# Performance work log

Hardware: AMD Instinct MI355X
Metric: run time of the kernel (lower is better)

The kernel has to match this reference:

```python
import jax, jax.numpy as jnp
import numpy as np

EPS = 1e-5

def setup_inputs() -> dict:
    key = jax.random.key(0)
    k1, k2, k3, k4, k5 = jax.random.split(key, 5)
    B, D, S = 4096, 2048, 16384
    return {
        "x": jax.random.normal(k1, (B, D), dtype=jnp.float32),
        "W_enc": jax.random.normal(k2, (S, D), dtype=jnp.float32) * 0.02,  # encoder.weight [n_sae, n_input]
        "W_dec": jax.random.normal(k3, (D, S), dtype=jnp.float32) * 0.02,  # decoder.weight [n_input, n_sae]
        "pre_bias": jax.random.normal(k4, (D,), dtype=jnp.float32) * 0.01,
        "sae_bias": jax.random.normal(k5, (S,), dtype=jnp.float32) * 0.01,
        "k": 64,
    }

def reference(x, W_enc, W_dec, pre_bias, sae_bias, k):
    # --- pre_process: layer norm (torch.std is unbiased -> ddof=1) ---
    x_mean = jnp.mean(x, axis=-1, keepdims=True)
    std = jnp.std(x, axis=-1, ddof=1, keepdims=True)
    x_ln = (x - x_mean) / (std + EPS)
    # --- encode: latents_pre = (x_ln - pre_bias) @ W_enc^T + sae_bias ---
    pre_activations = (x_ln - pre_bias) @ W_enc.T + sae_bias  # [B, n_sae]
    # --- TopK activation: keep top-k, ReLU them, zero the rest ---
    vals, idx = jax.lax.top_k(pre_activations, k)              # [B, k]
    vals = jax.nn.relu(vals)
    rows = jnp.arange(pre_activations.shape[0])[:, None]       # [B, 1]
    latents = jnp.zeros_like(pre_activations).at[rows, idx].set(vals)
    # --- decode + un-normalize ---
    recons = latents @ W_dec.T + pre_bias                      # [B, n_input]
    recons = recons * std + x_mean
    return pre_activations, latents, recons
```

## Files before the change

kernel.cpp:

```cpp
#include <hip/hip_runtime.h>
#include <cstdint>
#include <cstddef>

#define EPSV 1e-5f
#define CAP 224
#define PAD 16
#define DELTA 0.02f
#define AMBCAP 64

__device__ __forceinline__ unsigned short f2bf(float f) {
  unsigned u = __float_as_uint(f);
  unsigned r = (u + 0x7FFFu + ((u >> 16) & 1u)) >> 16;
  return (unsigned short)r;
}
__device__ __forceinline__ float bf2f(unsigned short h) {
  return __uint_as_float(((unsigned)h) << 16);
}

__global__ __launch_bounds__(256) void ln_kernel(const float* __restrict__ x,
    const float* __restrict__ pre_bias, float* __restrict__ a,
    unsigned short* __restrict__ A2,
    float* __restrict__ stats, int D) {
  const int b = blockIdx.x;
  const int tid = threadIdx.x;
  const float4* x4 = reinterpret_cast<const float4*>(x + (size_t)b * D);
  const float4* pb4 = reinterpret_cast<const float4*>(pre_bias);
  float4* a4 = reinterpret_cast<float4*>(a + (size_t)b * D);
  float4 v0 = x4[tid], v1 = x4[tid + 256];
  float s = v0.x + v0.y + v0.z + v0.w + v1.x + v1.y + v1.z + v1.w;
  float ss = v0.x*v0.x + v0.y*v0.y + v0.z*v0.z + v0.w*v0.w
           + v1.x*v1.x + v1.y*v1.y + v1.z*v1.z + v1.w*v1.w;
#pragma unroll
  for (int off = 1; off < 64; off <<= 1) { s += __shfl_xor(s, off); ss += __shfl_xor(ss, off); }
  __shared__ float wsum[4], wssq[4], bmean, bstd;
  int wave = tid >> 6;
  if ((tid & 63) == 0) { wsum[wave] = s; wssq[wave] = ss; }
  __syncthreads();
  if (tid == 0) {
    float S1 = wsum[0] + wsum[1] + wsum[2] + wsum[3];
    float S2 = wssq[0] + wssq[1] + wssq[2] + wssq[3];
    float mean = S1 / (float)D;
    float var = (S2 - (float)D * mean * mean) / (float)(D - 1);
    float sd = sqrtf(fmaxf(var, 0.f));
    bmean = mean; bstd = sd;
    stats[2*b] = mean; stats[2*b+1] = sd;
  }
  __syncthreads();
  float mean = bmean, rstd = 1.f / (bstd + EPSV);
  float4 p0 = pb4[tid], p1 = pb4[tid + 256];
  float4 o0, o1;
  o0.x = (v0.x - mean) * rstd - p0.x; o0.y = (v0.y - mean) * rstd - p0.y;
  o0.z = (v0.z - mean) * rstd - p0.z; o0.w = (v0.w - mean) * rstd - p0.w;
  o1.x = (v1.x - mean) * rstd - p1.x; o1.y = (v1.y - mean) * rstd - p1.y;
  o1.z = (v1.z - mean) * rstd - p1.z; o1.w = (v1.w - mean) * rstd - p1.w;
  a4[tid] = o0; a4[tid + 256] = o1;
  if (A2) {
    unsigned short* row = A2 + (size_t)b * 2048;
    ushort4 h0 = make_ushort4(f2bf(o0.x), f2bf(o0.y), f2bf(o0.z), f2bf(o0.w));
    ushort4 h1 = make_ushort4(f2bf(o1.x), f2bf(o1.y), f2bf(o1.z), f2bf(o1.w));
    *reinterpret_cast<ushort4*>(row + tid * 4) = h0;
    *reinterpret_cast<ushort4*>(row + 1024 + tid * 4) = h1;
  }
}

__global__ __launch_bounds__(256) void cvt_w_kernel(const float* __restrict__ W,
    unsigned short* __restrict__ W2, int D) {
  const int s = blockIdx.x, tid = threadIdx.x;
  const float4* w4 = reinterpret_cast<const float4*>(W + (size_t)s * D);
  unsigned short* row = W2 + (size_t)s * D;
  float4 v0 = w4[tid * 2], v1 = w4[tid * 2 + 1];
  uint4 p;
  p.x = (unsigned)f2bf(v0.x) | ((unsigned)f2bf(v0.y) << 16);
  p.y = (unsigned)f2bf(v0.z) | ((unsigned)f2bf(v0.w) << 16);
  p.z = (unsigned)f2bf(v1.x) | ((unsigned)f2bf(v1.y) << 16);
  p.w = (unsigned)f2bf(v1.z) | ((unsigned)f2bf(v1.w) << 16);
  *reinterpret_cast<uint4*>(row + tid * 8) = p;
}

typedef __attribute__((ext_vector_type(8))) short bf8;
typedef __attribute__((ext_vector_type(4))) float f32x4;

__device__ __forceinline__ void gload16(const void* g, void* l) {
  __builtin_amdgcn_global_load_lds(
      (const __attribute__((address_space(1))) unsigned int*)g,
      (__attribute__((address_space(3))) unsigned int*)l,
      16, 0, 0);
}

__global__ __launch_bounds__(256) void enc_gemm_bf16(
    const unsigned short* __restrict__ A2,
    const unsigned short* __restrict__ W2,
    const float* __restrict__ sae_bias,
    float* __restrict__ C, int M, int N) {
  __shared__ __align__(16) short As[128 * 64];
  __shared__ __align__(16) short Bs[128 * 64];
  const int tid = threadIdx.x;
  const int bn = blockIdx.x, bm = blockIdx.y;
  const int w = tid >> 6, l = tid & 63;

  const int lrow = l >> 3;
  const int lcol = ((l & 7) ^ lrow) * 8;
  const unsigned short* gA[4];
  const unsigned short* gB[4];
#pragma unroll
  for (int i = 0; i < 4; ++i) {
    int chunk = w * 4 + i;
    int row = chunk * 8 + lrow;
    gA[i] = A2 + (size_t)(bm * 128 + row) * 2048 + lcol;
    gB[i] = W2 + (size_t)(bn * 128 + row) * 2048 + lcol;
  }

  const int wm = (w >> 1) * 64, wn = (w & 1) * 64;
  const int r15 = l & 15, b7 = l & 7, u = l >> 4;
  const int colks0 = ((u + 0) ^ b7) * 8;
  const int colks1 = ((u + 4) ^ b7) * 8;
  const int baseA = (wm + r15) * 64;
  const int baseB = (wn + r15) * 64;

  f32x4 acc[4][4];
#pragma unroll
  for (int mi = 0; mi < 4; ++mi)
#pragma unroll
    for (int ni = 0; ni < 4; ++ni) acc[mi][ni] = (f32x4){0.f, 0.f, 0.f, 0.f};

  for (int t = 0; t < 32; ++t) {
    int koff = t * 64;
#pragma unroll
    for (int i = 0; i < 4; ++i) {
      int chunk = w * 4 + i;
      gload16(gA[i] + koff, &As[chunk * 512]);
      gload16(gB[i] + koff, &Bs[chunk * 512]);
    }
    __syncthreads();
#pragma unroll
    for (int ks = 0; ks < 2; ++ks) {
      const int ck = ks ? colks1 : colks0;
      bf8 af[4], bfv[4];
#pragma unroll
      for (int mi = 0; mi < 4; ++mi)
        af[mi] = *reinterpret_cast<const bf8*>(&As[baseA + mi * 1024 + ck]);
#pragma unroll
      for (int ni = 0; ni < 4; ++ni)
        bfv[ni] = *reinterpret_cast<const bf8*>(&Bs[baseB + ni * 1024 + ck]);
#pragma unroll
      for (int mi = 0; mi < 4; ++mi)
#pragma unroll
        for (int ni = 0; ni < 4; ++ni)
          acc[mi][ni] = __builtin_amdgcn_mfma_f32_16x16x32_bf16(
              af[mi], bfv[ni], acc[mi][ni], 0, 0, 0);
    }
    __syncthreads();
  }

  const int cm = (l >> 4) * 4, cn = l & 15;
  float sb[4];
#pragma unroll
  for (int ni = 0; ni < 4; ++ni)
    sb[ni] = sae_bias[bn * 128 + wn + ni * 16 + cn];
#pragma unroll
  for (int mi = 0; mi < 4; ++mi) {
#pragma unroll
    for (int r = 0; r < 4; ++r) {
      int row = bm * 128 + wm + mi * 16 + cm + r;
      float* Crow = C + (size_t)row * N + bn * 128 + wn;
#pragma unroll
      for (int ni = 0; ni < 4; ++ni)
        Crow[ni * 16 + cn] = acc[mi][ni][r] + sb[ni];
    }
  }
}

#define BM 128
#define BN 128
#define BK 32
#define LDP 136

__global__ __launch_bounds__(256) void enc_gemm_f32(
    const float* __restrict__ A, const float* __restrict__ Bw,
    const float* __restrict__ sae_bias, float* __restrict__ C,
    int M, int N, int K) {
  __shared__ __align__(16) float As[BK * LDP];
  __shared__ __align__(16) float Bs[BK * LDP];
  const int tid = threadIdx.x;
  const int bn = blockIdx.x, bm = blockIdx.y;
  const float* Ab = A + (size_t)bm * BM * K;
  const float* Bb = Bw + (size_t)bn * BN * K;
  float acc[8][8];
#pragma unroll
  for (int i = 0; i < 8; ++i)
#pragma unroll
    for (int j = 0; j < 8; ++j) acc[i][j] = 0.f;
  const int tn = tid & 15, tm = tid >> 4;
  const int lk = tid & 31;
  const int lm4 = (tid >> 5) * 4;
  for (int k0 = 0; k0 < K; k0 += BK) {
#pragma unroll
    for (int i = 0; i < 4; ++i) {
      int mb = i * 32 + lm4;
      float a0 = Ab[(size_t)(mb + 0) * K + k0 + lk];
      float a1 = Ab[(size_t)(mb + 1) * K + k0 + lk];
      float a2 = Ab[(size_t)(mb + 2) * K + k0 + lk];
      float a3 = Ab[(size_t)(mb + 3) * K + k0 + lk];
      *reinterpret_cast<float4*>(&As[lk * LDP + mb]) = make_float4(a0, a1, a2, a3);
      float b0 = Bb[(size_t)(mb + 0) * K + k0 + lk];
      float b1 = Bb[(size_t)(mb + 1) * K + k0 + lk];
      float b2 = Bb[(size_t)(mb + 2) * K + k0 + lk];
      float b3 = Bb[(size_t)(mb + 3) * K + k0 + lk];
      *reinterpret_cast<float4*>(&Bs[lk * LDP + mb]) = make_float4(b0, b1, b2, b3);
    }
    __syncthreads();
#pragma unroll 8
    for (int kk = 0; kk < BK; ++kk) {
      float4 a0 = *reinterpret_cast<const float4*>(&As[kk * LDP + tm * 4]);
      float4 a1 = *reinterpret_cast<const float4*>(&As[kk * LDP + tm * 4 + 64]);
      float4 b0 = *reinterpret_cast<const float4*>(&Bs[kk * LDP + tn * 4]);
      float4 b1 = *reinterpret_cast<const float4*>(&Bs[kk * LDP + tn * 4 + 64]);
      float av[8] = {a0.x, a0.y, a0.z, a0.w, a1.x, a1.y, a1.z, a1.w};
      float bv[8] = {b0.x, b0.y, b0.z, b0.w, b1.x, b1.y, b1.z, b1.w};
#pragma unroll
      for (int ii = 0; ii < 8; ++ii)
#pragma unroll
        for (int jj = 0; jj < 8; ++jj)
          acc[ii][jj] = fmaf(av[ii], bv[jj], acc[ii][jj]);
    }
    __syncthreads();
  }
  float4 sb0 = *reinterpret_cast<const float4*>(sae_bias + bn * BN + tn * 4);
  float4 sb1 = *reinterpret_cast<const float4*>(sae_bias + bn * BN + tn * 4 + 64);
#pragma unroll
  for (int ii = 0; ii < 8; ++ii) {
    int row = bm * BM + (ii < 4 ? tm * 4 + ii : 64 + tm * 4 + ii - 4);
    float* Crow = C + (size_t)row * N + bn * BN;
    float4 o0 = make_float4(acc[ii][0] + sb0.x, acc[ii][1] + sb0.y,
                            acc[ii][2] + sb0.z, acc[ii][3] + sb0.w);
    float4 o1 = make_float4(acc[ii][4] + sb1.x, acc[ii][5] + sb1.y,
                            acc[ii][6] + sb1.z, acc[ii][7] + sb1.w);
    *reinterpret_cast<float4*>(Crow + tn * 4) = o0;
    *reinterpret_cast<float4*>(Crow + tn * 4 + 64) = o1;
  }
}

__device__ __forceinline__ unsigned mapf(float f) {
  unsigned u = __float_as_uint(f);
  return (u & 0x80000000u) ? ~u : (u | 0x80000000u);
}

__global__ __launch_bounds__(256) void topk_select(
    const float* __restrict__ preact, float* __restrict__ latents,
    const int* __restrict__ kp, int* __restrict__ cand, float* __restrict__ candv,
    int* __restrict__ candcnt, int S) {
  const int b = blockIdx.x, tid = threadIdx.x;
  const float4* row4 = reinterpret_cast<const float4*>(preact + (size_t)b * S);
  __shared__ int hist[4096];
  __shared__ int tsum[256];
  __shared__ unsigned sh_pref, sh_thr;
  __shared__ int sh_done, sh_cum, sh_cnt;
  int K = kp[0]; if (K > 192) K = 192;
  const int r = K + PAD;
  if (tid == 0) { sh_done = 0; sh_pref = 0; sh_cum = 0; }
  for (int level = 0; level < 3; ++level) {
    __syncthreads();
    if (sh_done) break;
    const int shift = (level == 0) ? 20 : (level == 1) ? 8 : 0;
    const int width = (level == 2) ? 8 : 12;
    const int nb = 1 << width;
    const unsigned mask = (unsigned)nb - 1;
    for (int i = tid; i < nb; i += 256) hist[i] = 0;
    __syncthreads();
    const unsigned pref = sh_pref;
    for (int i = tid; i < S / 4; i += 256) {
      float4 v = row4[i];
      unsigned uu[4] = {mapf(v.x), mapf(v.y), mapf(v.z), mapf(v.w)};
#pragma unroll
      for (int q = 0; q < 4; ++q) {
        bool ok = (level == 0) || ((uu[q] >> (shift + width)) == pref);
        if (ok) atomicAdd(&hist[(uu[q] >> shift) & mask], 1);
      }
    }
    __syncthreads();
    const int per = nb >> 8;
    int myts = 0;
#pragma unroll 4
    for (int j = 0; j < per; ++j) myts += hist[tid * per + j];
    tsum[tid] = myts;
    __syncthreads();
    for (int o = 1; o < 256; o <<= 1) {
      int v_ = (tid + o < 256) ? tsum[tid + o] : 0;
      __syncthreads();
      tsum[tid] += v_;
      __syncthreads();
    }
    const int rr = r - sh_cum;
    const int sufIncl = tsum[tid];
    const int sufExcl = sufIncl - myts;
    if (sufExcl < rr && rr <= sufIncl) {
      int running = sufExcl;
      for (int j = per - 1; j >= 0; --j) {
        int bb = tid * per + j;
        int c = hist[bb];
        if (running + c >= rr) {
          unsigned npref = (sh_pref << width) | (unsigned)bb;
          int candTotal = sh_cum + running + c;
          sh_pref = npref;
          sh_cum += running;
          if (candTotal <= CAP || level == 2) { sh_thr = npref << shift; sh_done = 1; }
          break;
        }
        running += c;
      }
    }
  }
  __syncthreads();
  const unsigned T = sh_thr;
  if (tid == 0) sh_cnt = 0;
  __syncthreads();
  float4* lat4 = reinterpret_cast<float4*>(latents + (size_t)b * S);
  float4 z = make_float4(0.f, 0.f, 0.f, 0.f);
  for (int i = tid; i < S / 4; i += 256) {
    float4 v = row4[i];
    unsigned uu[4] = {mapf(v.x), mapf(v.y), mapf(v.z), mapf(v.w)};
    float vv[4] = {v.x, v.y, v.z, v.w};
#pragma unroll
    for (int q = 0; q < 4; ++q) {
      if (uu[q] >= T) {
        int p = atomicAdd(&sh_cnt, 1);
        if (p < CAP) { cand[(size_t)b * CAP + p] = i * 4 + q; candv[(size_t)b * CAP + p] = vv[q]; }
      }
    }
    lat4[i] = z;
  }
  __syncthreads();
  if (tid == 0) candcnt[b] = (sh_cnt < CAP) ? sh_cnt : CAP;
}

__global__ __launch_bounds__(256) void topk_refine(
    const float* __restrict__ a, const float* __restrict__ W_enc,
    const float* __restrict__ sae_bias, const int* __restrict__ kp,
    const int* __restrict__ cand, const float* __restrict__ candv,
    const int* __restrict__ candcnt,
    float* __restrict__ latents, int* __restrict__ out_idx, float* __restrict__ out_val,
    int D, int S) {
  const int b = blockIdx.x, tid = threadIdx.x;
  __shared__ float sv[256];
  __shared__ int si[256];
  __shared__ double sv64[256];
  __shared__ double av[AMBCAP];
  __shared__ int aslot[AMBCAP], agid[AMBCAP];
  __shared__ int sh_amb, sh_nin;
  int K = kp[0]; if (K > 192) K = 192;
  const int cnt = candcnt[b];
  const int wave = tid >> 6, lane = tid & 63;
  const float4* ar4 = reinterpret_cast<const float4*>(a + (size_t)b * D);
  const int nit = D / 256;

  if (tid < cnt) { sv[tid] = candv[(size_t)b * CAP + tid]; si[tid] = cand[(size_t)b * CAP + tid]; }
  else { sv[tid] = -3.0e38f; si[tid] = 0x7FFFFFFF; }
  __syncthreads();
  for (int ksz = 2; ksz <= 256; ksz <<= 1) {
    for (int j = ksz >> 1; j > 0; j >>= 1) {
      int ixj = tid ^ j;
      if (ixj > tid) {
        float v1 = sv[tid], v2 = sv[ixj];
        int i1 = si[tid], i2 = si[ixj];
        bool dirDesc = ((tid & ksz) == 0);
        bool firstBetter = (v1 > v2) || (v1 == v2 && i1 < i2);
        if (dirDesc ? (!firstBetter) : firstBetter) {
          sv[tid] = v2; sv[ixj] = v1; si[tid] = i2; si[ixj] = i1;
        }
      }
      __syncthreads();
    }
  }
  const float vK = sv[K - 1];
  if (tid == 0) { sh_amb = 0; sh_nin = 0; }
  __syncthreads();
  bool isC = tid < cnt;
  if (isC && (sv[tid] > vK + DELTA)) atomicAdd(&sh_nin, 1);
  if (isC && fabsf(sv[tid] - vK) <= DELTA) {
    int p = atomicAdd(&sh_amb, 1);
    if (p < AMBCAP) { aslot[p] = tid; agid[p] = si[tid]; }
  }
  __syncthreads();
  const int nAmb = sh_amb, nIn = sh_nin;

  if (nAmb <= AMBCAP) {
    for (int c = wave; c < nAmb; c += 4) {
      int sidx = agid[c];
      const float4* wr4 = reinterpret_cast<const float4*>(W_enc + (size_t)sidx * D);
      double acc = 0.0;
      for (int m = 0; m < nit; ++m) {
        float4 a_ = ar4[m * 64 + lane];
        float4 w_ = wr4[m * 64 + lane];
        acc += (double)a_.x * w_.x + (double)a_.y * w_.y
             + (double)a_.z * w_.z + (double)a_.w * w_.w;
      }
#pragma unroll
      for (int off = 1; off < 64; off <<= 1) acc += __shfl_xor(acc, off);
      if (lane == 0) av[c] = acc + (double)sae_bias[sidx];
    }
    __syncthreads();
    if (tid < AMBCAP && tid >= nAmb) { av[tid] = -1.0e300; agid[tid] = 0x7FFFFFFF; }
    __syncthreads();
    for (int ksz = 2; ksz <= AMBCAP; ksz <<= 1) {
      for (int j = ksz >> 1; j > 0; j >>= 1) {
        int ixj = tid ^ j;
        if (tid < AMBCAP && ixj > tid) {
          double v1 = av[tid], v2 = av[ixj];
          int i1 = agid[tid], i2 = agid[ixj];
          bool dirDesc = ((tid & ksz) == 0);
          bool firstBetter = (v1 > v2) || (v1 == v2 && i1 < i2);
          if (dirDesc ? (!firstBetter) : firstBetter) {
            av[tid] = v2; av[ixj] = v1; agid[tid] = i2; agid[ixj] = i1;
          }
        }
        __syncthreads();
      }
    }
    if (tid < K) {
      int gidx; float val;
      if (tid < nIn) { gidx = si[tid]; val = sv[tid]; }
      else { int c = tid - nIn; gidx = agid[c]; val = (float)av[c]; }
      val = fmaxf(val, 0.f);
      latents[(size_t)b * S + gidx] = val;
      out_idx[(size_t)b * 256 + tid] = gidx;
      out_val[(size_t)b * 256 + tid] = val;
    }
  } else {
    for (int c = wave; c < cnt; c += 4) {
      int sidx = si[c];
      const float4* wr4 = reinterpret_cast<const float4*>(W_enc + (size_t)sidx * D);
      double acc = 0.0;
      for (int m = 0; m < nit; ++m) {
        float4 a_ = ar4[m * 64 + lane];
        float4 w_ = wr4[m * 64 + lane];
        acc += (double)a_.x * w_.x + (double)a_.y * w_.y
             + (double)a_.z * w_.z + (double)a_.w * w_.w;
      }
#pragma unroll
      for (int off = 1; off < 64; off <<= 1) acc += __shfl_xor(acc, off);
      if (lane == 0) sv64[c] = acc + (double)sae_bias[sidx];
    }
    __syncthreads();
    if (tid >= cnt) { sv64[tid] = -1.0e300; si[tid] = 0x7FFFFFFF; }
    __syncthreads();
    for (int ksz = 2; ksz <= 256; ksz <<= 1) {
      for (int j = ksz >> 1; j > 0; j >>= 1) {
        int ixj = tid ^ j;
        if (ixj > tid) {
          double v1 = sv64[tid], v2 = sv64[ixj];
          int i1 = si[tid], i2 = si[ixj];
          bool dirDesc = ((tid & ksz) == 0);
          bool firstBetter = (v1 > v2) || (v1 == v2 && i1 < i2);
          if (dirDesc ? (!firstBetter) : firstBetter) {
            sv64[tid] = v2; sv64[ixj] = v1; si[tid] = i2; si[ixj] = i1;
          }
        }
        __syncthreads();
      }
    }
    if (tid < K) {
      int idx = si[tid];
      float rv = fmaxf((float)sv64[tid], 0.f);
      latents[(size_t)b * S + idx] = rv;
      out_idx[(size_t)b * 256 + tid] = idx;
      out_val[(size_t)b * 256 + tid] = rv;
    }
  }
}

__global__ __launch_bounds__(256) void transpose_cvt(const float* __restrict__ src,
    unsigned short* __restrict__ dst, int D, int S) {
  __shared__ float t[32][33];
  int s0 = blockIdx.x * 32, d0 = blockIdx.y * 32;
  int tx = threadIdx.x & 31, ty = threadIdx.x >> 5;
#pragma unroll
  for (int i = 0; i < 32; i += 8)
    t[ty + i][tx] = src[(size_t)(d0 + ty + i) * S + s0 + tx];
  __syncthreads();
#pragma unroll
  for (int i = 0; i < 32; i += 8)
    dst[(size_t)(s0 + ty + i) * D + d0 + tx] = f2bf(t[tx][ty + i]);
}

__global__ __launch_bounds__(256) void decode_bf16(
    const unsigned short* __restrict__ WdTh, const float* __restrict__ pre_bias,
    const float* __restrict__ stats, const int* __restrict__ kp,
    const int* __restrict__ out_idx, const float* __restrict__ out_val,
    float* __restrict__ recons, int D) {
  const int b = blockIdx.x, tid = threadIdx.x;
  __shared__ int sidx[192];
  __shared__ float sval[192];
  int K = kp[0]; if (K > 192) K = 192;
  if (tid < K) { sidx[tid] = out_idx[(size_t)b * 256 + tid]; sval[tid] = out_val[(size_t)b * 256 + tid]; }
  __syncthreads();
  const int c0 = tid * 8;
  float4 p0 = *reinterpret_cast<const float4*>(pre_bias + c0);
  float4 p1 = *reinterpret_cast<const float4*>(pre_bias + c0 + 4);
  float acc[8] = {p0.x, p0.y, p0.z, p0.w, p1.x, p1.y, p1.z, p1.w};
  for (int j = 0; j < K; ++j) {
    float v = sval[j];
    uint4 wv = *reinterpret_cast<const uint4*>(WdTh + (size_t)sidx[j] * D + c0);
    acc[0] = fmaf(v, bf2f((unsigned short)(wv.x & 0xffff)), acc[0]);
    acc[1] = fmaf(v, bf2f((unsigned short)(wv.x >> 16)),    acc[1]);
    acc[2] = fmaf(v, bf2f((unsigned short)(wv.y & 0xffff)), acc[2]);
    acc[3] = fmaf(v, bf2f((unsigned short)(wv.y >> 16)),    acc[3]);
    acc[4] = fmaf(v, bf2f((unsigned short)(wv.z & 0xffff)), acc[4]);
    acc[5] = fmaf(v, bf2f((unsigned short)(wv.z >> 16)),    acc[5]);
    acc[6] = fmaf(v, bf2f((unsigned short)(wv.w & 0xffff)), acc[6]);
    acc[7] = fmaf(v, bf2f((unsigned short)(wv.w >> 16)),    acc[7]);
  }
  float mean = stats[2 * b], sd = stats[2 * b + 1];
  float4 o0 = make_float4(acc[0] * sd + mean, acc[1] * sd + mean,
                          acc[2] * sd + mean, acc[3] * sd + mean);
  float4 o1 = make_float4(acc[4] * sd + mean, acc[5] * sd + mean,
                          acc[6] * sd + mean, acc[7] * sd + mean);
  float* r = recons + (size_t)b * D + c0;
  *reinterpret_cast<float4*>(r) = o0;
  *reinterpret_cast<float4*>(r + 4) = o1;
}

__global__ __launch_bounds__(256) void decode_fb(
    const float* __restrict__ Wd, const float* __restrict__ pre_bias,
    const float* __restrict__ stats, const int* __restrict__ kp,
    const int* __restrict__ out_idx, const float* __restrict__ out_val,
    float* __restrict__ recons, int D, int S) {
  const int b = blockIdx.x, tid = threadIdx.x;
  __shared__ int sidx[192];
  __shared__ float sval[192];
  int K = kp[0]; if (K > 192) K = 192;
  if (tid < K) { sidx[tid] = out_idx[(size_t)b * 256 + tid]; sval[tid] = out_val[(size_t)b * 256 + tid]; }
  __syncthreads();
  for (int d = tid; d < D; d += 256) {
    float acc = pre_bias[d];
    for (int j = 0; j < K; ++j)
      acc = fmaf(sval[j], Wd[(size_t)d * S + sidx[j]], acc);
    recons[(size_t)b * D + d] = acc * stats[2 * b + 1] + stats[2 * b];
  }
}

extern "C" void kernel_launch(void* const* d_in, const int* in_sizes, int n_in,
                              void* d_out, int out_size, void* d_ws, size_t ws_size,
                              hipStream_t stream) {
  const float* x        = (const float*)d_in[0];
  const float* W_enc    = (const float*)d_in[1];
  const float* W_dec    = (const float*)d_in[2];
  const float* pre_bias = (const float*)d_in[3];
  const float* sae_bias = (const float*)d_in[4];
  const int*   kp       = (const int*)d_in[5];
  const int D = in_sizes[3];
  const int S = in_sizes[4];
  const int B = in_sizes[0] / D;

  float* out_pre = (float*)d_out;
  float* out_lat = out_pre + (size_t)B * S;
  float* out_rec = out_lat + (size_t)B * S;

  char* ws = (char*)d_ws;
  size_t off = 0;
  float* a = (float*)(ws + off);        off += (size_t)B * D * 4;
  float* stats = (float*)(ws + off);    off += (size_t)B * 2 * 4;
  int* cand = (int*)(ws + off);         off += (size_t)B * CAP * 4;
  float* candv = (float*)(ws + off);    off += (size_t)B * CAP * 4;
  int* candcnt = (int*)(ws + off);      off += (size_t)B * 4;
  int* oidx = (int*)(ws + off);         off += (size_t)B * 256 * 4;
  float* oval = (float*)(ws + off);     off += (size_t)B * 256 * 4;
  off = (off + 255) & ~(size_t)255;
  unsigned short* A2 = (unsigned short*)(ws + off);
  size_t offW2 = off + (size_t)B * D * 2;
  unsigned short* W2 = (unsigned short*)(ws + offW2);
  size_t offWdT = offW2 + (size_t)S * D * 2;
  unsigned short* WdTh = (unsigned short*)(ws + offWdT);
  size_t offEnd = offWdT + (size_t)S * D * 2;
  bool useBf16 = (D == 2048) && (B % 128 == 0) && (S % 128 == 0) &&
                 (S % 32 == 0) && (D % 32 == 0) && (ws_size >= offEnd);

  if (useBf16) {
    ln_kernel<<<B, 256, 0, stream>>>(x, pre_bias, a, A2, stats, D);
    cvt_w_kernel<<<S, 256, 0, stream>>>(W_enc, W2, D);
    enc_gemm_bf16<<<dim3(S / 128, B / 128), 256, 0, stream>>>(A2, W2, sae_bias, out_pre, B, S);
    transpose_cvt<<<dim3(S / 32, D / 32), 256, 0, stream>>>(W_dec, WdTh, D, S);
    topk_select<<<B, 256, 0, stream>>>(out_pre, out_lat, kp, cand, candv, candcnt, S);
    topk_refine<<<B, 256, 0, stream>>>(a, W_enc, sae_bias, kp, cand, candv, candcnt,
                                       out_lat, oidx, oval, D, S);
    decode_bf16<<<B, 256, 0, stream>>>(WdTh, pre_bias, stats, kp, oidx, oval, out_rec, D);
  } else {
    ln_kernel<<<B, 256, 0, stream>>>(x, pre_bias, a, nullptr, stats, D);
    enc_gemm_f32<<<dim3(S / BN, B / BM), 256, 0, stream>>>(a, W_enc, sae_bias, out_pre, B, S, D);
    topk_select<<<B, 256, 0, stream>>>(out_pre, out_lat, kp, cand, candv, candcnt, S);
    topk_refine<<<B, 256, 0, stream>>>(a, W_enc, sae_bias, kp, cand, candv, candcnt,
                                       out_lat, oidx, oval, D, S);
    decode_fb<<<B, 256, 0, stream>>>(W_dec, pre_bias, stats, kp, oidx, oval, out_rec, D, S);
  }
}
```

Baseline: 916.9 us.

## Double-buffer LDS tiles in encoder GEMM to overlap global loads with MFMA

The encoder bf16 GEMM now uses two LDS buffer pairs. It issues the global-to-LDS loads for the next K tile before computing on the current one, so load latency overlaps with MFMA work and each tile needs only one barrier instead of two. It also raises wave priority around the MFMA block with s_setprio. The cost is doubled LDS use (64KB per block), which may reduce occupancy, and the explicit vmcnt(0) wait plus barrier must order the buffer reuse correctly.

```diff
diff --git a/kernel.cpp b/kernel.cpp
--- a/kernel.cpp
+++ b/kernel.cpp
@@ -92,8 +92,10 @@
     const unsigned short* __restrict__ W2,
     const float* __restrict__ sae_bias,
     float* __restrict__ C, int M, int N) {
-  __shared__ __align__(16) short As[128 * 64];
-  __shared__ __align__(16) short Bs[128 * 64];
+  __shared__ __align__(16) short As0[128 * 64];
+  __shared__ __align__(16) short Bs0[128 * 64];
+  __shared__ __align__(16) short As1[128 * 64];
+  __shared__ __align__(16) short Bs1[128 * 64];
   const int tid = threadIdx.x;
   const int bn = blockIdx.x, bm = blockIdx.y;
   const int w = tid >> 6, l = tid & 63;
@@ -109,6 +111,7 @@
     gA[i] = A2 + (size_t)(bm * 128 + row) * 2048 + lcol;
     gB[i] = W2 + (size_t)(bn * 128 + row) * 2048 + lcol;
   }
+  const int ldsOff = (w * 4) * 512 + l * 8;
 
   const int wm = (w >> 1) * 64, wn = (w & 1) * 64;
   const int r15 = l & 15, b7 = l & 7, u = l >> 4;
@@ -123,34 +126,59 @@
 #pragma unroll
     for (int ni = 0; ni < 4; ++ni) acc[mi][ni] = (f32x4){0.f, 0.f, 0.f, 0.f};
 
-  for (int t = 0; t < 32; ++t) {
-    int koff = t * 64;
-#pragma unroll
-    for (int i = 0; i < 4; ++i) {
-      int chunk = w * 4 + i;
-      gload16(gA[i] + koff, &As[chunk * 512]);
-      gload16(gB[i] + koff, &Bs[chunk * 512]);
-    }
-    __syncthreads();
-#pragma unroll
-    for (int ks = 0; ks < 2; ++ks) {
-      const int ck = ks ? colks1 : colks0;
-      bf8 af[4], bfv[4];
-#pragma unroll
-      for (int mi = 0; mi < 4; ++mi)
-        af[mi] = *reinterpret_cast<const bf8*>(&As[baseA + mi * 1024 + ck]);
-#pragma unroll
-      for (int ni = 0; ni < 4; ++ni)
-        bfv[ni] = *reinterpret_cast<const bf8*>(&Bs[baseB + ni * 1024 + ck]);
-#pragma unroll
-      for (int mi = 0; mi < 4; ++mi)
-#pragma unroll
-        for (int ni = 0; ni < 4; ++ni)
-          acc[mi][ni] = __builtin_amdgcn_mfma_f32_16x16x32_bf16(
-              af[mi], bfv[ni], acc[mi][ni], 0, 0, 0);
-    }
-    __syncthreads();
-  }
+#define STAGE(Adst, Bdst, koff)                                   \
+  {                                                               \
+    _Pragma("unroll")                                             \
+    for (int i = 0; i < 4; ++i) {                                 \
+      gload16(gA[i] + (koff), &(Adst)[ldsOff + i * 512]);         \
+      gload16(gB[i] + (koff), &(Bdst)[ldsOff + i * 512]);         \
+    }                                                             \
+  }
+
+#define COMPUTE(Asrc, Bsrc)                                       \
+  {                                                               \
+    _Pragma("unroll")                                             \
+    for (int ks = 0; ks < 2; ++ks) {                              \
+      const int ck = ks ? colks1 : colks0;                        \
+      bf8 af[4], bfv[4];                                          \
+      _Pragma("unroll")                                           \
+      for (int mi = 0; mi < 4; ++mi)                              \
+        af[mi] = *reinterpret_cast<const bf8*>(&(Asrc)[baseA + mi * 1024 + ck]); \
+      _Pragma("unroll")                                           \
+      for (int ni = 0; ni < 4; ++ni)                              \
+        bfv[ni] = *reinterpret_cast<const bf8*>(&(Bsrc)[baseB + ni * 1024 + ck]); \
+      __builtin_amdgcn_s_setprio(1);                              \
+      _Pragma("unroll")                                           \
+      for (int mi = 0; mi < 4; ++mi)                              \
+        _Pragma("unroll")                                         \
+        for (int ni = 0; ni < 4; ++ni)                            \
+          acc[mi][ni] = __builtin_amdgcn_mfma_f32_16x16x32_bf16(  \
+              af[mi], bfv[ni], acc[mi][ni], 0, 0, 0);             \
+      __builtin_amdgcn_s_setprio(0);                              \
+    }                                                             \
+  }
+
+#define SYNC_TILE()                                               \
+  {                                                               \
+    asm volatile("s_waitcnt vmcnt(0)" ::: "memory");              \
+    __builtin_amdgcn_s_barrier();                                 \
+    asm volatile("" ::: "memory");                                \
+  }
+
+  STAGE(As0, Bs0, 0);
+  SYNC_TILE();
+
+  for (int t = 0; t < 32; t += 2) {
+    STAGE(As1, Bs1, (t + 1) * 64);
+    COMPUTE(As0, Bs0);
+    SYNC_TILE();
+    if (t + 2 < 32) STAGE(As0, Bs0, (t + 2) * 64);
+    COMPUTE(As1, Bs1);
+    SYNC_TILE();
+  }
+#undef STAGE
+#undef COMPUTE
+#undef SYNC_TILE
 
   const int cm = (l >> 4) * 4, cn = l & 15;
   float sb[4];
```

Result: faster. 862.2 us (-6.0%).
